# Kernel tuning notes

Measured on AMD Instinct MI355X. Metric: run time of the kernel, lower is better.

## Reference

```python
import jax, jax.numpy as jnp
import numpy as np

B, T, E, D = 8, 2048, 1024, 128  # batch, seq, embedding_dim, head_dim


def setup_inputs() -> dict:
    key = jax.random.key(0)
    ks = jax.random.split(key, 7)
    s = 1.0 / np.sqrt(E)  # torch Linear default init scale
    return {
        "x": jax.random.normal(ks[0], (B, T, E), dtype=jnp.float32),
        "Wq": jax.random.uniform(ks[1], (E, D), jnp.float32, -s, s),
        "bq": jax.random.uniform(ks[2], (D,), jnp.float32, -s, s),
        "Wk": jax.random.uniform(ks[3], (E, D), jnp.float32, -s, s),
        "bk": jax.random.uniform(ks[4], (D,), jnp.float32, -s, s),
        "Wv": jax.random.uniform(ks[5], (E, D), jnp.float32, -s, s),
        "bv": jax.random.uniform(ks[6], (D,), jnp.float32, -s, s),
        "mask": 1,
    }


def reference(x, Wq, bq, Wk, bk, Wv, bv, mask):
    # Q/K/V projections: [B,T,E] @ [E,D] -> [B,T,D]
    q = x @ Wq + bq
    k = x @ Wk + bk
    v = x @ Wv + bv
    d_k = q.shape[-1]
    # scores: [B,T,T]
    scores = jnp.einsum("btd,bsd->bts", q, k) / jnp.sqrt(jnp.float32(d_k))
    if mask:  # causal masked_fill with -inf (static python flag)
        causal = jnp.tril(jnp.ones((q.shape[1], q.shape[1]), dtype=bool))
        scores = jnp.where(causal[None, :, :], scores, -jnp.inf)
    att = jax.nn.softmax(scores, axis=-1)
    # dropout p=0.0 (inference) -> identity
    return jnp.einsum("bts,bsd->btd", att, v)
```

## Files before the change

### kernel.cpp

```cpp
#include <hip/hip_runtime.h>
#include <hip/hip_bf16.h>

#define BSZ  8
#define TSEQ 2048
#define EDIM 1024
#define DDIM 128
#define MROWS (BSZ * TSEQ)
#define NQT  (TSEQ / 64)

typedef __attribute__((ext_vector_type(8))) __bf16 bf16x8;
typedef __attribute__((ext_vector_type(4))) __bf16 bf16x4;
typedef __attribute__((ext_vector_type(2))) __bf16 bf16x2;
typedef __attribute__((ext_vector_type(4))) float f32x4;

__global__ __launch_bounds__(256) void wt_kernel(
    const float* __restrict__ Wq, const float* __restrict__ Wk,
    const float* __restrict__ Wv, __bf16* __restrict__ wt)
{
    const float* W = (blockIdx.y == 0) ? Wq : (blockIdx.y == 1) ? Wk : Wv;
    __bf16* o = wt + (size_t)blockIdx.y * DDIM * EDIM;
    const int k0 = blockIdx.x * 64;
    __shared__ __align__(16) __bf16 t[64][140];
    const int tid = threadIdx.x;
    #pragma unroll
    for (int i = 0; i < 8; ++i) {
        int idx = tid + i * 256;
        int k = idx >> 5, c4 = idx & 31;
        float4 v = *(const float4*)&W[(size_t)(k0 + k) * DDIM + c4 * 4];
        bf16x4 b4;
        b4[0] = (__bf16)v.x; b4[1] = (__bf16)v.y; b4[2] = (__bf16)v.z; b4[3] = (__bf16)v.w;
        *(bf16x4*)&t[k][c4 * 4] = b4;
    }
    __syncthreads();
    #pragma unroll
    for (int i = 0; i < 4; ++i) {
        int idx = tid + i * 256;
        int n = idx >> 3, c8 = idx & 7;
        bf16x8 r;
        #pragma unroll
        for (int u = 0; u < 8; ++u) r[u] = t[c8 * 8 + u][n];
        *(bf16x8*)&o[(size_t)n * EDIM + k0 + c8 * 8] = r;
    }
}

__global__ __launch_bounds__(256) void qkv_fused_kernel(
    const float* __restrict__ x, const __bf16* __restrict__ wt,
    const float* __restrict__ bq, const float* __restrict__ bk,
    const float* __restrict__ bv,
    __bf16* __restrict__ qo, __bf16* __restrict__ ko, __bf16* __restrict__ vto)
{
    const int m0 = (blockIdx.x >> 1) * 64;
    const int h  = blockIdx.x & 1;

    __shared__ __align__(16) __bf16 a_lds[64][72];
    __shared__ __align__(16) __bf16 b_lds[192][72];

    const int tid  = threadIdx.x;
    const int lane = tid & 63;
    const int wv   = tid >> 6;
    const int wr   = wv >> 1, wc = wv & 1;
    const int cl   = lane & 15, gr = lane >> 4;

    f32x4 acc[2][6] = {};

    float4 ra[4];
    bf16x8 rb[6];
    const int arow = tid >> 4,  ac4 = tid & 15;
    const int brow = tid >> 3,  bc8 = tid & 7;

#define LOADAB(K0) do {                                                        \
    _Pragma("unroll")                                                          \
    for (int i = 0; i < 4; ++i)                                                \
        ra[i] = *(const float4*)&x[(size_t)(m0 + arow + i * 16) * EDIM + (K0) + ac4 * 4]; \
    _Pragma("unroll")                                                          \
    for (int i = 0; i < 6; ++i)                                                \
        rb[i] = *(const bf16x8*)&wt[(size_t)(h * 192 + brow + i * 32) * EDIM + (K0) + bc8 * 8]; \
  } while (0)

    LOADAB(0);

    for (int k0 = 0; k0 < EDIM; k0 += 64) {
        #pragma unroll
        for (int i = 0; i < 4; ++i) {
            bf16x4 b4;
            b4[0] = (__bf16)ra[i].x; b4[1] = (__bf16)ra[i].y;
            b4[2] = (__bf16)ra[i].z; b4[3] = (__bf16)ra[i].w;
            *(bf16x4*)&a_lds[arow + i * 16][ac4 * 4] = b4;
        }
        #pragma unroll
        for (int i = 0; i < 6; ++i)
            *(bf16x8*)&b_lds[brow + i * 32][bc8 * 8] = rb[i];
        __syncthreads();

        if (k0 + 64 < EDIM) LOADAB(k0 + 64);

        #pragma unroll
        for (int ks = 0; ks < 2; ++ks) {
            bf16x8 af[2], bfr[6];
            #pragma unroll
            for (int mi = 0; mi < 2; ++mi)
                af[mi] = *(const bf16x8*)&a_lds[wr * 32 + mi * 16 + cl][ks * 32 + gr * 8];
            #pragma unroll
            for (int ni = 0; ni < 6; ++ni)
                bfr[ni] = *(const bf16x8*)&b_lds[wc * 96 + ni * 16 + cl][ks * 32 + gr * 8];
            #pragma unroll
            for (int mi = 0; mi < 2; ++mi)
                #pragma unroll
                for (int ni = 0; ni < 6; ++ni)
                    acc[mi][ni] = __builtin_amdgcn_mfma_f32_16x16x32_bf16(
                        af[mi], bfr[ni], acc[mi][ni], 0, 0, 0);
        }
        __syncthreads();
    }
#undef LOADAB

    const float qsc = 0.08838834764831845f;
    #pragma unroll
    for (int ni = 0; ni < 6; ++ni) {
        const int nbase = h * 192 + wc * 96 + ni * 16;
        const int which = nbase >> 7;
        const int d     = (nbase & 127) + cl;
        const float* bias = (which == 0) ? bq : (which == 1) ? bk : bv;
        const float bb = bias[d];
        const float sc = (which == 0) ? qsc : 1.0f;
        #pragma unroll
        for (int mi = 0; mi < 2; ++mi) {
            const int row = m0 + wr * 32 + mi * 16 + gr * 4;
            if (which == 2) {
                bf16x4 p;
                #pragma unroll
                for (int r = 0; r < 4; ++r) p[r] = (__bf16)(acc[mi][ni][r] + bb);
                *(bf16x4*)&vto[(size_t)d * MROWS + row] = p;
            } else {
                __bf16* o = (which == 0) ? qo : ko;
                #pragma unroll
                for (int r = 0; r < 4; ++r)
                    o[(size_t)(row + r) * DDIM + d] = (__bf16)((acc[mi][ni][r] + bb) * sc);
            }
        }
    }
}

__global__ __launch_bounds__(256, 3) void attn_partial_kernel(
    const __bf16* __restrict__ Q, const __bf16* __restrict__ K,
    const __bf16* __restrict__ Vt,
    __bf16* __restrict__ partO, float* __restrict__ partM, float* __restrict__ partL,
    int PL, int NP)
{
    const int bid = blockIdx.x;
    const int b   = blockIdx.y;

    int g = 0, rem = bid;
    for (;;) {
        const int np_g = (g + 1 + PL - 1) / PL;
        if (rem < np_g) break;
        rem -= np_g; ++g;
    }
    const int qt = g, p = rem;
    const int tiles = qt + 1;
    const int np = (tiles + PL - 1) / PL;
    const int lb = tiles / np, ex = tiles % np;
    const int mylen = lb + (p < ex);
    const int start = p * lb + min(p, ex);
    const int kv_lo = start * 64;
    const int kv_hi = kv_lo + mylen * 64;

    __shared__ __align__(16) __bf16 k_lds[64][136];
    __shared__ __align__(16) __bf16 v_lds[128][72];
    __shared__ __align__(16) __bf16 p_lds[4][16][72];

    const int tid  = threadIdx.x;
    const int lane = tid & 63;
    const int w    = tid >> 6;
    const int cl   = lane & 15, gr = lane >> 4;

    const int qrow = qt * 64 + w * 16;
    const size_t bT = (size_t)b * TSEQ;

    bf16x8 qf[4];
    const __bf16* qbase = Q + (bT + qrow + cl) * DDIM;
    #pragma unroll
    for (int ks = 0; ks < 4; ++ks)
        qf[ks] = *(const bf16x8*)&qbase[ks * 32 + gr * 8];

    f32x4 acc[8] = {};
    float m1 = -__builtin_inff();
    float l1 = 0.f;

    bf16x8 rk[4], rv[4];
#define LOAD_TILE(KV0) do {                                                   \
    _Pragma("unroll")                                                         \
    for (int i = 0; i < 4; ++i) {                                             \
        int idx = tid + i * 256;                                              \
        rk[i] = *(const bf16x8*)&K[(bT + (KV0) + (idx >> 4)) * DDIM + (idx & 15) * 8]; } \
    _Pragma("unroll")                                                         \
    for (int i = 0; i < 4; ++i) {                                             \
        int idx = tid + i * 256;                                              \
        rv[i] = *(const bf16x8*)&Vt[(size_t)(idx >> 3) * MROWS + bT + (KV0) + (idx & 7) * 8]; } \
  } while (0)

    LOAD_TILE(kv_lo);

    for (int kv0 = kv_lo; kv0 < kv_hi; kv0 += 64) {
        #pragma unroll
        for (int i = 0; i < 4; ++i) {
            int idx = tid + i * 256;
            *(bf16x8*)&k_lds[idx >> 4][(idx & 15) * 8] = rk[i];
        }
        #pragma unroll
        for (int i = 0; i < 4; ++i) {
            int idx = tid + i * 256;
            *(bf16x8*)&v_lds[idx >> 3][(idx & 7) * 8] = rv[i];
        }
        __syncthreads();

        if (kv0 + 64 < kv_hi) LOAD_TILE(kv0 + 64);

        f32x4 s[4] = {};
        #pragma unroll
        for (int ks = 0; ks < 4; ++ks) {
            #pragma unroll
            for (int st = 0; st < 4; ++st) {
                bf16x8 kf = *(const bf16x8*)&k_lds[st * 16 + cl][ks * 32 + gr * 8];
                s[st] = __builtin_amdgcn_mfma_f32_16x16x32_bf16(kf, qf[ks], s[st], 0, 0, 0);
            }
        }

        if (kv0 + 63 > qrow) {
            const int kvb = kv0 + gr * 4 - qrow - cl;
            #pragma unroll
            for (int st = 0; st < 4; ++st)
                #pragma unroll
                for (int r = 0; r < 4; ++r)
                    if (kvb + st * 16 + r > 0) s[st][r] = -__builtin_inff();
        }

        float tm = fmaxf(fmaxf(fmaxf(s[0][0], s[0][1]), fmaxf(s[0][2], s[0][3])),
                         fmaxf(fmaxf(s[1][0], s[1][1]), fmaxf(s[1][2], s[1][3])));
        tm = fmaxf(tm,
             fmaxf(fmaxf(fmaxf(s[2][0], s[2][1]), fmaxf(s[2][2], s[2][3])),
                   fmaxf(fmaxf(s[3][0], s[3][1]), fmaxf(s[3][2], s[3][3]))));
        tm = fmaxf(tm, __shfl_xor(tm, 16));
        tm = fmaxf(tm, __shfl_xor(tm, 32));

        if (__any(tm > m1)) {
            const float newm = fmaxf(m1, tm);
            const float alpha = __expf(m1 - newm);
            l1 *= alpha;
            m1 = newm;
            float arec[4];
            #pragma unroll
            for (int r = 0; r < 4; ++r) arec[r] = __shfl(alpha, gr * 4 + r);
            #pragma unroll
            for (int d = 0; d < 8; ++d) {
                #pragma unroll
                for (int r = 0; r < 4; ++r) acc[d][r] *= arec[r];
            }
        }

        #pragma unroll
        for (int st = 0; st < 4; ++st) {
            #pragma unroll
            for (int u = 0; u < 2; ++u) {
                float p0 = __expf(s[st][2 * u]     - m1);
                float p1 = __expf(s[st][2 * u + 1] - m1);
                l1 += p0 + p1;
                bf16x2 pp; pp[0] = (__bf16)p0; pp[1] = (__bf16)p1;
                *(bf16x2*)&p_lds[w][cl][st * 16 + gr * 4 + 2 * u] = pp;
            }
        }

        #pragma unroll
        for (int ks2 = 0; ks2 < 2; ++ks2) {
            bf16x8 pa = *(const bf16x8*)&p_lds[w][cl][ks2 * 32 + gr * 8];
            #pragma unroll
            for (int d = 0; d < 8; ++d) {
                bf16x8 vf = *(const bf16x8*)&v_lds[d * 16 + cl][ks2 * 32 + gr * 8];
                acc[d] = __builtin_amdgcn_mfma_f32_16x16x32_bf16(pa, vf, acc[d], 0, 0, 0);
            }
        }
        __syncthreads();
    }
#undef LOAD_TILE

    const size_t pidx = (size_t)b * NP + bid;
    __bf16* po = partO + pidx * (64 * 128);
    float ls = l1;
    ls += __shfl_xor(ls, 16);
    ls += __shfl_xor(ls, 32);
    if (gr == 0) {
        partM[pidx * 64 + w * 16 + cl] = m1;
        partL[pidx * 64 + w * 16 + cl] = ls;
    }
    #pragma unroll
    for (int r = 0; r < 4; ++r) {
        const int row_l = w * 16 + gr * 4 + r;
        #pragma unroll
        for (int d = 0; d < 8; ++d)
            po[row_l * 128 + d * 16 + cl] = (__bf16)acc[d][r];
    }
}

__global__ __launch_bounds__(256) void attn_combine_kernel(
    const __bf16* __restrict__ partO, const float* __restrict__ partM,
    const float* __restrict__ partL, float* __restrict__ out, int PL, int NP)
{
    const int qt = blockIdx.x, b = blockIdx.y;
    int pre = 0;
    for (int g2 = 0; g2 < qt; ++g2) pre += (g2 + 1 + PL - 1) / PL;
    const int nv = (qt + 1 + PL - 1) / PL;
    const size_t pbase = (size_t)b * NP + pre;

    const int tid = threadIdx.x;
    const int col = (tid & 31) * 4;
    const int rbase = blockIdx.z * 32;

    #pragma unroll
    for (int rr = 0; rr < 4; ++rr) {
        const int row = rbase + (tid >> 5) + rr * 8;
        float mx = -__builtin_inff();
        for (int c = 0; c < nv; ++c)
            mx = fmaxf(mx, partM[(pbase + c) * 64 + row]);
        float lsum = 0.f;
        f32x4 o = {0.f, 0.f, 0.f, 0.f};
        for (int c = 0; c < nv; ++c) {
            const float wgt = __expf(partM[(pbase + c) * 64 + row] - mx);
            lsum += wgt * partL[(pbase + c) * 64 + row];
            const bf16x4 po = *(const bf16x4*)&partO[(pbase + c) * (64 * 128) + (size_t)row * 128 + col];
            o.x += wgt * (float)po[0]; o.y += wgt * (float)po[1];
            o.z += wgt * (float)po[2]; o.w += wgt * (float)po[3];
        }
        const float inv = 1.0f / lsum;
        f32x4 res = {o.x * inv, o.y * inv, o.z * inv, o.w * inv};
        *(f32x4*)&out[((size_t)b * TSEQ + qt * 64 + row) * DDIM + col] = res;
    }
}

extern "C" void kernel_launch(void* const* d_in, const int* in_sizes, int n_in,
                              void* d_out, int out_size, void* d_ws, size_t ws_size,
                              hipStream_t stream) {
    const float* x  = (const float*)d_in[0];
    const float* Wq = (const float*)d_in[1];
    const float* bq = (const float*)d_in[2];
    const float* Wk = (const float*)d_in[3];
    const float* bk = (const float*)d_in[4];
    const float* Wv = (const float*)d_in[5];
    const float* bv = (const float*)d_in[6];

    __bf16* q  = (__bf16*)d_ws;
    __bf16* k  = q  + (size_t)MROWS * DDIM;
    __bf16* vt = k  + (size_t)MROWS * DDIM;
    __bf16* wt = vt + (size_t)MROWS * DDIM;
    const size_t fixed_bytes = ((size_t)3 * MROWS * DDIM + (size_t)3 * DDIM * EDIM) * sizeof(__bf16);

    int PL = 4, NP = 0;
    for (int g2 = 0; g2 < NQT; ++g2) NP += (g2 + 1 + PL - 1) / PL;
    {
        const size_t need = fixed_bytes +
            (size_t)NP * BSZ * 64 * (128 * sizeof(__bf16) + 2 * sizeof(float));
        if (ws_size < need) {
            PL = 8; NP = 0;
            for (int g2 = 0; g2 < NQT; ++g2) NP += (g2 + 1 + PL - 1) / PL;
        }
    }
    __bf16* partO = (__bf16*)((char*)d_ws + fixed_bytes);
    float* partM = (float*)(partO + (size_t)NP * BSZ * 64 * 128);
    float* partL = partM + (size_t)NP * BSZ * 64;

    wt_kernel<<<dim3(EDIM / 64, 3), 256, 0, stream>>>(Wq, Wk, Wv, wt);
    qkv_fused_kernel<<<dim3((MROWS / 64) * 2), 256, 0, stream>>>(x, wt, bq, bk, bv, q, k, vt);
    attn_partial_kernel<<<dim3(NP, BSZ), 256, 0, stream>>>(q, k, vt, partO, partM, partL, PL, NP);
    attn_combine_kernel<<<dim3(NQT, BSZ, 2), 256, 0, stream>>>(partO, partM, partL,
                                                               (float*)d_out, PL, NP);
}
```

Measured before the change: 85.16 us.

## Load QKV projection fragments directly from global memory, dropping LDS staging

The QKV projection GEMM stops staging x and the transposed weights through shared memory. Each lane now loads its MFMA fragments straight from global memory, removes both barriers per k-step, and sets a two-blocks-per-CU launch bound. Block indices are remapped so the two N-halves of the same M tile land on the same XCD and can share L2. In exchange, global loads become uncoalesced 16-32 byte per-lane reads, and each x row is fetched by both wave columns without reuse through LDS.

Result: slower. 133.5 us (+56.7%).

```diff
diff --git a/kernel.cpp b/kernel.cpp
--- a/kernel.cpp
+++ b/kernel.cpp
@@ -43,17 +43,17 @@
     }
 }
 
-__global__ __launch_bounds__(256) void qkv_fused_kernel(
+__global__ __launch_bounds__(256, 2) void qkv_fused_kernel(
     const float* __restrict__ x, const __bf16* __restrict__ wt,
     const float* __restrict__ bq, const float* __restrict__ bk,
     const float* __restrict__ bv,
     __bf16* __restrict__ qo, __bf16* __restrict__ ko, __bf16* __restrict__ vto)
 {
-    const int m0 = (blockIdx.x >> 1) * 64;
-    const int h  = blockIdx.x & 1;
-
-    __shared__ __align__(16) __bf16 a_lds[64][72];
-    __shared__ __align__(16) __bf16 b_lds[192][72];
+    const int bid = blockIdx.x;
+    const int xcd = bid & 7;
+    const int nt  = (bid >> 3) & 1;
+    const int mt  = (bid >> 4) * 8 + xcd;
+    const int m0  = mt * 64;
 
     const int tid  = threadIdx.x;
     const int lane = tid & 63;
@@ -63,61 +63,58 @@
 
     f32x4 acc[2][6] = {};
 
-    float4 ra[4];
-    bf16x8 rb[6];
-    const int arow = tid >> 4,  ac4 = tid & 15;
-    const int brow = tid >> 3,  bc8 = tid & 7;
-
-#define LOADAB(K0) do {                                                        \
-    _Pragma("unroll")                                                          \
-    for (int i = 0; i < 4; ++i)                                                \
-        ra[i] = *(const float4*)&x[(size_t)(m0 + arow + i * 16) * EDIM + (K0) + ac4 * 4]; \
-    _Pragma("unroll")                                                          \
-    for (int i = 0; i < 6; ++i)                                                \
-        rb[i] = *(const bf16x8*)&wt[(size_t)(h * 192 + brow + i * 32) * EDIM + (K0) + bc8 * 8]; \
-  } while (0)
-
-    LOADAB(0);
-
+    const float* abase[2];
+    #pragma unroll
+    for (int mi = 0; mi < 2; ++mi)
+        abase[mi] = x + (size_t)(m0 + wr * 32 + mi * 16 + cl) * EDIM + gr * 8;
+    const __bf16* bbase[6];
+    #pragma unroll
+    for (int ni = 0; ni < 6; ++ni)
+        bbase[ni] = wt + (size_t)(nt * 192 + wc * 96 + ni * 16 + cl) * EDIM + gr * 8;
+
+    #pragma unroll 2
     for (int k0 = 0; k0 < EDIM; k0 += 64) {
-        #pragma unroll
-        for (int i = 0; i < 4; ++i) {
-            bf16x4 b4;
-            b4[0] = (__bf16)ra[i].x; b4[1] = (__bf16)ra[i].y;
-            b4[2] = (__bf16)ra[i].z; b4[3] = (__bf16)ra[i].w;
-            *(bf16x4*)&a_lds[arow + i * 16][ac4 * 4] = b4;
-        }
-        #pragma unroll
-        for (int i = 0; i < 6; ++i)
-            *(bf16x8*)&b_lds[brow + i * 32][bc8 * 8] = rb[i];
-        __syncthreads();
-
-        if (k0 + 64 < EDIM) LOADAB(k0 + 64);
+        f32x4 ar[2][2][2];
+        #pragma unroll
+        for (int mi = 0; mi < 2; ++mi)
+            #pragma unroll
+            for (int ks = 0; ks < 2; ++ks) {
+                ar[mi][ks][0] = *(const f32x4*)(abase[mi] + k0 + ks * 32);
+                ar[mi][ks][1] = *(const f32x4*)(abase[mi] + k0 + ks * 32 + 4);
+            }
+        bf16x8 br[6][2];
+        #pragma unroll
+        for (int ni = 0; ni < 6; ++ni)
+            #pragma unroll
+            for (int ks = 0; ks < 2; ++ks)
+                br[ni][ks] = *(const bf16x8*)(bbase[ni] + k0 + ks * 32);
 
         #pragma unroll
         for (int ks = 0; ks < 2; ++ks) {
-            bf16x8 af[2], bfr[6];
-            #pragma unroll
-            for (int mi = 0; mi < 2; ++mi)
-                af[mi] = *(const bf16x8*)&a_lds[wr * 32 + mi * 16 + cl][ks * 32 + gr * 8];
-            #pragma unroll
-            for (int ni = 0; ni < 6; ++ni)
-                bfr[ni] = *(const bf16x8*)&b_lds[wc * 96 + ni * 16 + cl][ks * 32 + gr * 8];
+            bf16x8 af[2];
+            #pragma unroll
+            for (int mi = 0; mi < 2; ++mi) {
+                bf16x8 t;
+                #pragma unroll
+                for (int u = 0; u < 4; ++u) {
+                    t[u]     = (__bf16)ar[mi][ks][0][u];
+                    t[u + 4] = (__bf16)ar[mi][ks][1][u];
+                }
+                af[mi] = t;
+            }
             #pragma unroll
             for (int mi = 0; mi < 2; ++mi)
                 #pragma unroll
                 for (int ni = 0; ni < 6; ++ni)
                     acc[mi][ni] = __builtin_amdgcn_mfma_f32_16x16x32_bf16(
-                        af[mi], bfr[ni], acc[mi][ni], 0, 0, 0);
-        }
-        __syncthreads();
-    }
-#undef LOADAB
+                        af[mi], br[ni][ks], acc[mi][ni], 0, 0, 0);
+        }
+    }
 
     const float qsc = 0.08838834764831845f;
     #pragma unroll
     for (int ni = 0; ni < 6; ++ni) {
-        const int nbase = h * 192 + wc * 96 + ni * 16;
+        const int nbase = nt * 192 + wc * 96 + ni * 16;
         const int which = nbase >> 7;
         const int d     = (nbase & 127) + cl;
         const float* bias = (which == 0) ? bq : (which == 1) ? bk : bv;
@@ -368,7 +365,7 @@
     float* partL = partM + (size_t)NP * BSZ * 64;
 
     wt_kernel<<<dim3(EDIM / 64, 3), 256, 0, stream>>>(Wq, Wk, Wv, wt);
-    qkv_fused_kernel<<<dim3((MROWS / 64) * 2), 256, 0, stream>>>(x, wt, bq, bk, bv, q, k, vt);
+    qkv_fused_kernel<<<dim3(MROWS / 64 * 2), 256, 0, stream>>>(x, wt, bq, bk, bv, q, k, vt);
     attn_partial_kernel<<<dim3(NP, BSZ), 256, 0, stream>>>(q, k, vt, partO, partM, partL, PL, NP);
     attn_combine_kernel<<<dim3(NQT, BSZ, 2), 256, 0, stream>>>(partO, partM, partL,
                                                                (float*)d_out, PL, NP);
```
